# Performance work log

Hardware: AMD Instinct MI355X
Metric: run time of the kernel (lower is better)

## Reference

```python
import jax, jax.numpy as jnp
import numpy as np

B1, B2, CHUNK, HID, T = 64, 16, 128, 64, 131072
N_CHUNKS = 128


def setup_inputs() -> dict:
    key = jax.random.key(0)
    ks = jax.random.split(key, 12)
    # positive prices so log(p) is finite
    p = jax.random.uniform(ks[0], (T, 2), jnp.float32) * 2.0 + 0.5
    inds = jax.random.randint(ks[1], (B1,), 0, 100000, dtype=jnp.int32)
    open_slices = jax.random.randint(ks[2], (B1, B2, 1), 0, T, dtype=jnp.int32)
    ls_probs = jax.random.uniform(ks[3], (B1, B2, 1, 1), jnp.float32)
    open_probs = jax.random.uniform(ks[4], (B1, B2, 1, 1), jnp.float32)
    open_hx = jax.random.normal(ks[5], (B1, B2, 2, HID), jnp.float32) * 0.1
    s = 1.0 / np.sqrt(HID)
    # torch nn.LSTM params: gate order i,f,g,o
    W_ih = jax.random.uniform(ks[6], (4 * HID, 2), jnp.float32, -s, s)
    W_hh = jax.random.uniform(ks[7], (4 * HID, HID), jnp.float32, -s, s)
    b_ih = jax.random.uniform(ks[8], (4 * HID,), jnp.float32, -s, s)
    b_hh = jax.random.uniform(ks[9], (4 * HID,), jnp.float32, -s, s)
    W_out = jax.random.uniform(ks[10], (1, HID), jnp.float32, -s, s)
    b_out = jax.random.uniform(ks[11], (1,), jnp.float32, -s, s)
    return {"inds": inds, "p": p, "ls_probs": ls_probs, "open_probs": open_probs,
            "open_slices": open_slices, "open_hx": open_hx,
            "W_ih": W_ih, "W_hh": W_hh, "b_ih": b_ih, "b_hh": b_hh,
            "W_out": W_out, "b_out": b_out, "n_chunks": N_CHUNKS}


def reference(inds, p, ls_probs, open_probs, open_slices, open_hx,
              W_ih, W_hh, b_ih, b_hh, W_out, b_out, n_chunks):
    b1, b2 = open_hx.shape[:2]
    hid = open_hx.shape[-1]
    C = CHUNK
    h0 = open_hx[:, :, 0, :].reshape(b1 * b2, hid)
    c0 = open_hx[:, :, 1, :].reshape(b1 * b2, hid)
    open_logp = jnp.log(p[open_slices])  # (b1, b2, 1, 2)
    # sliding-window gather base: idx[i,j,t] = inds[i] + j + t (per-chunk offset added in scan)
    base = (inds[:, None, None]
            + jnp.arange(b2, dtype=inds.dtype)[None, :, None]
            + jnp.arange(C, dtype=inds.dtype)[None, None, :])  # (b1, b2, C)
    bias = b_ih + b_hh

    def lstm_chunk(x, h, c):  # x: (N, C, 2)
        xg = x @ W_ih.T + bias  # precompute input projection: (N, C, 4H)
        def step(carry, xg_t):
            h, c = carry
            g = xg_t + h @ W_hh.T
            i, f, gg, o = jnp.split(g, 4, axis=-1)
            c = jax.nn.sigmoid(f) * c + jax.nn.sigmoid(i) * jnp.tanh(gg)
            h = jax.nn.sigmoid(o) * jnp.tanh(c)
            return (h, c), h
        (h, c), hs = jax.lax.scan(step, (h, c), xg.swapaxes(0, 1))
        return hs.swapaxes(0, 1), h, c  # (N, C, H)

    def chunk_step(carry, offset):
        h, c, last_nd, loss = carry
        idx = base + offset * C                      # (b1, b2, C)
        p_chunk = p[idx]                             # (b1, b2, C, 2)
        x = p_chunk - p_chunk[:, :, :1, :]           # re-center on first step of chunk
        out, h, c = lstm_chunk(x.reshape(b1 * b2, C, 2), h, c)
        probs = jax.nn.sigmoid(out.reshape(b1, b2, C, hid) @ W_out.T + b_out)  # (b1,b2,C,1)
        not_done = last_nd * jnp.cumprod(1.0 - probs[:, :, :-1], axis=2)       # (b1,b2,C-1,1)
        probs = jnp.concatenate([probs[:, :, :1], probs[:, :, 1:] * not_done], axis=2)
        last_nd = not_done[:, :, -1:, :]
        logp = jnp.log(p_chunk)
        payoff = ls_probs * (logp - open_logp) + (1.0 - ls_probs) * (open_logp - logp)
        loss = loss + jnp.sum(open_probs * probs * payoff)
        return (h, c, last_nd, loss), None

    init = (h0, c0, jnp.ones((b1, b2, 1, 1), p.dtype), jnp.zeros((), p.dtype))
    (_, _, _, loss), _ = jax.lax.scan(chunk_step, init, jnp.arange(n_chunks))
    return loss
```

## Files before the change

### kernel.cpp

```cpp
#include <hip/hip_runtime.h>


#define CH  128
#define HID 64

typedef __fp16 half8 __attribute__((ext_vector_type(8)));
typedef float  f32x4 __attribute__((ext_vector_type(4)));
typedef int    int4v __attribute__((ext_vector_type(4)));

__device__ __forceinline__ float rlf(float v, int l) {
  return __builtin_bit_cast(float, __builtin_amdgcn_readlane(__builtin_bit_cast(int, v), l));
}
__device__ __forceinline__ int packh(float a, float b) {
  return __builtin_bit_cast(int, __builtin_amdgcn_cvt_pkrtz(a, b));
}
__device__ __forceinline__ float frcp(float x) { return __builtin_amdgcn_rcpf(x); }
__device__ __forceinline__ float sigm(float x) { return frcp(1.0f + __expf(-x)); }
__device__ __forceinline__ float tanh_(float x) {
  float e = __expf(2.0f * x);
  return 1.0f - 2.0f * frcp(e + 1.0f);
}
template <int CTRL, int RMASK>
__device__ __forceinline__ float dpp_add(float v) {
  int x = __builtin_amdgcn_update_dpp(0, __builtin_bit_cast(int, v), CTRL, RMASK, 0xF, true);
  return v + __builtin_bit_cast(float, x);
}
__device__ __forceinline__ float dpp_xor1(float v) {
  int x = __builtin_amdgcn_update_dpp(0, __builtin_bit_cast(int, v), 0xB1, 0xF, 0xF, true);
  return __builtin_bit_cast(float, x);
}
__device__ __forceinline__ float dpp_wave_sum(float v) {
  v = dpp_add<0x111, 0xF>(v);
  v = dpp_add<0x112, 0xF>(v);
  v = dpp_add<0x114, 0xF>(v);
  v = dpp_add<0x118, 0xF>(v);
  v = dpp_add<0x142, 0xA>(v);
  v = dpp_add<0x143, 0xC>(v);
  return v;
}

__global__ __attribute__((amdgpu_flat_work_group_size(128, 128), amdgpu_waves_per_eu(2, 2)))
void pc_lstm_kernel(const int* __restrict__ inds,
                    const float* __restrict__ p,
                    const float* __restrict__ ls_probs,
                    const float* __restrict__ open_probs,
                    const int* __restrict__ open_slices,
                    const float* __restrict__ open_hx,
                    const float* __restrict__ W_ih,
                    const float* __restrict__ W_hh,
                    const float* __restrict__ b_ih,
                    const float* __restrict__ b_hh,
                    const float* __restrict__ W_out,
                    const float* __restrict__ b_out,
                    const int* __restrict__ n_chunks_p,
                    float* __restrict__ out)
{
  __shared__ __fp16 ring[2][CH][HID];
  __shared__ int prod;
  __shared__ int cons;

  const int tid  = threadIdx.x;
  const int wv   = tid >> 6;
  const int lane = tid & 63;
  const int s    = blockIdx.x;
  const int n_chunks = n_chunks_p[0];
  const int tbase = inds[s >> 4] + (s & 15);
  const float2* p2 = (const float2*)p;

  if (tid == 0) { prod = 0; cons = 0; }
  __syncthreads();

  if (wv == 0) {
    const int kg = lane >> 4;
    const int cc = lane & 15;

    half8 Wb[32];
#pragma unroll
    for (int t = 0; t < 16; ++t) {
#pragma unroll
      for (int kc = 0; kc < 2; ++kc) {
        const float* wp = W_hh + (16 * t + cc) * HID + 32 * kc + 8 * kg;
        half8 w;
#pragma unroll
        for (int j = 0; j < 8; ++j) w[j] = (__fp16)wp[j];
        Wb[2 * t + kc] = w;
      }
    }

    float wxa[4], wxb[4], bb[4];
#pragma unroll
    for (int g = 0; g < 4; ++g) {
      const int r = g * HID + lane;
      wxa[g] = W_ih[2 * r];
      wxb[g] = W_ih[2 * r + 1];
      bb[g]  = b_ih[r] + b_hh[r];
    }
    float h = open_hx[(s * 2 + 0) * HID + lane];
    float c = open_hx[(s * 2 + 1) * HID + lane];

    int ia0[4], ia1[4];
#pragma unroll
    for (int w = 0; w < 4; ++w) {
      ia0[w] = 4 * (8 * kg + 2 * w);
      ia1[w] = 4 * (32 + 8 * kg + 2 * w);
    }

    const bool u1 = (lane & 16) != 0;
    const bool u2 = (lane & 32) != 0;
    const f32x4 zero4 = {0.f, 0.f, 0.f, 0.f};

    float2 curA = p2[tbase + lane];
    float2 curB = p2[tbase + HID + lane];
    float2 nxtA = curA, nxtB = curB;

    for (int off = 0; off < n_chunks; ++off) {
      if (off) { curA = nxtA; curB = nxtB; }
      const float px0 = rlf(curA.x, 0);
      const float px1 = rlf(curA.y, 0);
      float2 xA, xB;
      xA.x = curA.x - px0; xA.y = curA.y - px1;
      xB.x = curB.x - px0; xB.y = curB.y - px1;
      if (off + 1 < n_chunks) {
        const int nb = tbase + (off + 1) * CH;
        nxtA = p2[nb + lane];
        nxtB = p2[nb + HID + lane];
      }
      while (__hip_atomic_load(&cons, __ATOMIC_ACQUIRE, __HIP_MEMORY_SCOPE_WORKGROUP) + 2 <= off)
        __builtin_amdgcn_s_sleep(8);

      __fp16* slot = &ring[off & 1][0][0];
#pragma unroll
      for (int hf = 0; hf < 2; ++hf) {
        const float xcx = hf ? xB.x : xA.x;
        const float xcy = hf ? xB.y : xA.y;
#pragma unroll 1
        for (int tl = 0; tl < 64; ++tl) {
          const int hp = packh(h, dpp_xor1(h));
          int4v A0, A1;
#pragma unroll
          for (int w = 0; w < 4; ++w) {
            A0[w] = __builtin_amdgcn_ds_bpermute(ia0[w], hp);
            A1[w] = __builtin_amdgcn_ds_bpermute(ia1[w], hp);
          }
          const half8 a0 = __builtin_bit_cast(half8, A0);
          const half8 a1 = __builtin_bit_cast(half8, A1);

          const float x0 = rlf(xcx, tl);
          const float x1 = rlf(xcy, tl);

          float pa[4];
#pragma unroll
          for (int g = 0; g < 4; ++g) {
            f32x4 q0 = __builtin_amdgcn_mfma_f32_16x16x32_f16(a0, Wb[8 * g + 0], zero4, 0, 0, 0);
            q0       = __builtin_amdgcn_mfma_f32_16x16x32_f16(a1, Wb[8 * g + 1], q0,    0, 0, 0);
            f32x4 q1 = __builtin_amdgcn_mfma_f32_16x16x32_f16(a0, Wb[8 * g + 2], zero4, 0, 0, 0);
            q1       = __builtin_amdgcn_mfma_f32_16x16x32_f16(a1, Wb[8 * g + 3], q1,    0, 0, 0);
            f32x4 q2 = __builtin_amdgcn_mfma_f32_16x16x32_f16(a0, Wb[8 * g + 4], zero4, 0, 0, 0);
            q2       = __builtin_amdgcn_mfma_f32_16x16x32_f16(a1, Wb[8 * g + 5], q2,    0, 0, 0);
            f32x4 q3 = __builtin_amdgcn_mfma_f32_16x16x32_f16(a0, Wb[8 * g + 6], zero4, 0, 0, 0);
            q3       = __builtin_amdgcn_mfma_f32_16x16x32_f16(a1, Wb[8 * g + 7], q3,    0, 0, 0);
            const float s01 = u1 ? q1[0] : q0[0];
            const float s23 = u1 ? q3[0] : q2[0];
            const float dg  = u2 ? s23 : s01;
            pa[g] = fmaf(x0, wxa[g], fmaf(x1, wxb[g], dg + bb[g]));
          }

          const float ig = sigm(pa[0]);
          const float fg = sigm(pa[1]);
          const float gg = tanh_(pa[2]);
          const float og = sigm(pa[3]);
          c = fmaf(fg, c, ig * gg);
          h = og * tanh_(c);

          const int tt = hf * 64 + tl;
          slot[tt * HID + lane] = (__fp16)h;
        }
      }
      if (lane == 0)
        __hip_atomic_store(&prod, off + 1, __ATOMIC_RELEASE, __HIP_MEMORY_SCOPE_WORKGROUP);
    }
  } else {
    const float wo   = W_out[lane];
    const float bout = b_out[0];
    const int   os   = open_slices[s];
    const float OL   = __logf(p[2 * os]) + __logf(p[2 * os + 1]);
    const float coef = open_probs[s] * (2.0f * ls_probs[s] - 1.0f);

    float S = 1.0f, D = 1.0f, lsum = 0.0f, psum = 0.0f;

    for (int off = 0; off < n_chunks; ++off) {
      const int cb = tbase + off * CH;
      const float2 cA = p2[cb + lane];
      const float2 cB = p2[cb + HID + lane];
      const float LA = __logf(cA.x) + __logf(cA.y);
      const float LB = __logf(cB.x) + __logf(cB.y);

      while (__hip_atomic_load(&prod, __ATOMIC_ACQUIRE, __HIP_MEMORY_SCOPE_WORKGROUP) <= off)
        __builtin_amdgcn_s_sleep(32);

      const __fp16* slot = &ring[off & 1][0][0];
#pragma unroll 1
      for (int tt = 0; tt < CH; ++tt) {
        const float hv = (float)slot[tt * HID + lane];
        const float z  = rlf(dpp_wave_sum(hv * wo), 63);
        const float pr = sigm(z + bout);
        const float Lt = (tt < 64) ? rlf(LA, tt) : rlf(LB, tt - 64);
        const float pn = (tt == 0) ? pr : pr * D;
        lsum = fmaf(pn, Lt, lsum);
        psum += pn;
        if (tt == 0)           D = S * (1.0f - pr);
        else if (tt < CH - 1)  D *= (1.0f - pr);
        else                   S = D;
      }
      if (lane == 0)
        __hip_atomic_store(&cons, off + 1, __ATOMIC_RELEASE, __HIP_MEMORY_SCOPE_WORKGROUP);
    }
    if (lane == 0) atomicAdd(out, coef * (lsum - OL * psum));
  }
}

extern "C" void kernel_launch(void* const* d_in, const int* in_sizes, int n_in,
                              void* d_out, int out_size, void* d_ws, size_t ws_size,
                              hipStream_t stream) {
  (void)hipMemsetAsync(d_out, 0, sizeof(float), stream);

  pc_lstm_kernel<<<dim3(1024), dim3(128), 0, stream>>>(
      (const int*)d_in[0],
      (const float*)d_in[1],
      (const float*)d_in[2],
      (const float*)d_in[3],
      (const int*)d_in[4],
      (const float*)d_in[5],
      (const float*)d_in[6],
      (const float*)d_in[7],
      (const float*)d_in[8],
      (const float*)d_in[9],
      (const float*)d_in[10],
      (const float*)d_in[11],
      (const int*)d_in[12],
      (float*)d_out);
}
```

Measured before the change: 7.032 ms.

## Split LSTM gate matmuls across both waves with per-step LDS handshakes

The recurrent W_hh matmul is now divided between the two waves. Wave 0 computes the input and cell gates. Wave 1 computes the forget and output gates and also evaluates the output head one step behind. The gate values and h are exchanged every timestep through LDS, using tag-encoded 64-bit slots and a step counter with spin-waits. This replaces the old chunk-level producer/consumer ring. The aim is to halve the serial MFMA chain per timestep, at the cost of two cross-wave LDS round trips and busy-waiting on the critical path of every step.

```diff
diff --git a/kernel.cpp b/kernel.cpp
--- a/kernel.cpp
+++ b/kernel.cpp
@@ -7,6 +7,8 @@
 typedef __fp16 half8 __attribute__((ext_vector_type(8)));
 typedef float  f32x4 __attribute__((ext_vector_type(4)));
 typedef int    int4v __attribute__((ext_vector_type(4)));
+
+#define MFMA16(A, B, C) __builtin_amdgcn_mfma_f32_16x16x32_f16((A), (B), (C), 0, 0, 0)
 
 __device__ __forceinline__ float rlf(float v, int l) {
   return __builtin_bit_cast(float, __builtin_amdgcn_readlane(__builtin_bit_cast(int, v), l));
@@ -37,6 +39,10 @@
   v = dpp_add<0x142, 0xA>(v);
   v = dpp_add<0x143, 0xC>(v);
   return v;
+}
+__device__ __forceinline__ unsigned long long enc_tag(float v, int gs) {
+  const unsigned b = __builtin_bit_cast(unsigned, v);
+  return (unsigned long long)b | ((unsigned long long)(b ^ (unsigned)gs) << 32);
 }
 
 __global__ __attribute__((amdgpu_flat_work_group_size(128, 128), amdgpu_waves_per_eu(2, 2)))
@@ -55,46 +61,48 @@
                     const int* __restrict__ n_chunks_p,
                     float* __restrict__ out)
 {
-  __shared__ __fp16 ring[2][CH][HID];
-  __shared__ int prod;
-  __shared__ int cons;
+  __shared__ __fp16 hring[4][HID];
+  __shared__ unsigned long long commF[HID];
+  __shared__ unsigned long long commO[HID];
+  __shared__ int hflag;
 
   const int tid  = threadIdx.x;
   const int wv   = tid >> 6;
   const int lane = tid & 63;
   const int s    = blockIdx.x;
   const int n_chunks = n_chunks_p[0];
+  const int NSTEP = n_chunks * CH;
   const int tbase = inds[s >> 4] + (s & 15);
   const float2* p2 = (const float2*)p;
-
-  if (tid == 0) { prod = 0; cons = 0; }
+  const int kg = lane >> 4;
+  const int cc = lane & 15;
+  const bool u1 = (lane & 16) != 0;
+  const bool u2 = (lane & 32) != 0;
+  const f32x4 zero4 = {0.f, 0.f, 0.f, 0.f};
+
+  if (tid < HID) { commF[tid] = 0ull; commO[tid] = 0ull; }
+  if (tid == 0) hflag = -1;
   __syncthreads();
 
   if (wv == 0) {
-    const int kg = lane >> 4;
-    const int cc = lane & 15;
-
-    half8 Wb[32];
-#pragma unroll
-    for (int t = 0; t < 16; ++t) {
+    half8 Wb[16];
+#pragma unroll
+    for (int ti = 0; ti < 8; ++ti) {
+      const int t = (ti < 4) ? ti : ti + 4;
 #pragma unroll
       for (int kc = 0; kc < 2; ++kc) {
         const float* wp = W_hh + (16 * t + cc) * HID + 32 * kc + 8 * kg;
         half8 w;
 #pragma unroll
         for (int j = 0; j < 8; ++j) w[j] = (__fp16)wp[j];
-        Wb[2 * t + kc] = w;
-      }
-    }
-
-    float wxa[4], wxb[4], bb[4];
-#pragma unroll
-    for (int g = 0; g < 4; ++g) {
-      const int r = g * HID + lane;
-      wxa[g] = W_ih[2 * r];
-      wxb[g] = W_ih[2 * r + 1];
-      bb[g]  = b_ih[r] + b_hh[r];
-    }
+        Wb[2 * ti + kc] = w;
+      }
+    }
+    const float wxi0 = W_ih[2 * lane],                wxi1 = W_ih[2 * lane + 1];
+    const float bbi  = b_ih[lane] + b_hh[lane];
+    const float wxg0 = W_ih[2 * (2 * HID + lane)],    wxg1 = W_ih[2 * (2 * HID + lane) + 1];
+    const float bbg  = b_ih[2 * HID + lane] + b_hh[2 * HID + lane];
+
     float h = open_hx[(s * 2 + 0) * HID + lane];
     float c = open_hx[(s * 2 + 1) * HID + lane];
 
@@ -105,9 +113,10 @@
       ia1[w] = 4 * (32 + 8 * kg + 2 * w);
     }
 
-    const bool u1 = (lane & 16) != 0;
-    const bool u2 = (lane & 32) != 0;
-    const f32x4 zero4 = {0.f, 0.f, 0.f, 0.f};
+    int hp = packh(h, dpp_xor1(h));
+    ((unsigned short*)&hring[0][0])[lane] = (unsigned short)(hp & 0xffff);
+    asm volatile("" ::: "memory");
+    __hip_atomic_store(&hflag, 0, __ATOMIC_RELAXED, __HIP_MEMORY_SCOPE_WORKGROUP);
 
     float2 curA = p2[tbase + lane];
     float2 curB = p2[tbase + HID + lane];
@@ -125,61 +134,96 @@
         nxtA = p2[nb + lane];
         nxtB = p2[nb + HID + lane];
       }
-      while (__hip_atomic_load(&cons, __ATOMIC_ACQUIRE, __HIP_MEMORY_SCOPE_WORKGROUP) + 2 <= off)
-        __builtin_amdgcn_s_sleep(8);
-
-      __fp16* slot = &ring[off & 1][0][0];
 #pragma unroll
       for (int hf = 0; hf < 2; ++hf) {
         const float xcx = hf ? xB.x : xA.x;
         const float xcy = hf ? xB.y : xA.y;
 #pragma unroll 1
         for (int tl = 0; tl < 64; ++tl) {
-          const int hp = packh(h, dpp_xor1(h));
+          const int gs = off * CH + hf * 64 + tl + 1;
           int4v A0, A1;
 #pragma unroll
-          for (int w = 0; w < 4; ++w) {
-            A0[w] = __builtin_amdgcn_ds_bpermute(ia0[w], hp);
-            A1[w] = __builtin_amdgcn_ds_bpermute(ia1[w], hp);
-          }
+          for (int w = 0; w < 4; ++w) A0[w] = __builtin_amdgcn_ds_bpermute(ia0[w], hp);
+#pragma unroll
+          for (int w = 0; w < 4; ++w) A1[w] = __builtin_amdgcn_ds_bpermute(ia1[w], hp);
           const half8 a0 = __builtin_bit_cast(half8, A0);
           const half8 a1 = __builtin_bit_cast(half8, A1);
-
           const float x0 = rlf(xcx, tl);
           const float x1 = rlf(xcy, tl);
 
-          float pa[4];
-#pragma unroll
-          for (int g = 0; g < 4; ++g) {
-            f32x4 q0 = __builtin_amdgcn_mfma_f32_16x16x32_f16(a0, Wb[8 * g + 0], zero4, 0, 0, 0);
-            q0       = __builtin_amdgcn_mfma_f32_16x16x32_f16(a1, Wb[8 * g + 1], q0,    0, 0, 0);
-            f32x4 q1 = __builtin_amdgcn_mfma_f32_16x16x32_f16(a0, Wb[8 * g + 2], zero4, 0, 0, 0);
-            q1       = __builtin_amdgcn_mfma_f32_16x16x32_f16(a1, Wb[8 * g + 3], q1,    0, 0, 0);
-            f32x4 q2 = __builtin_amdgcn_mfma_f32_16x16x32_f16(a0, Wb[8 * g + 4], zero4, 0, 0, 0);
-            q2       = __builtin_amdgcn_mfma_f32_16x16x32_f16(a1, Wb[8 * g + 5], q2,    0, 0, 0);
-            f32x4 q3 = __builtin_amdgcn_mfma_f32_16x16x32_f16(a0, Wb[8 * g + 6], zero4, 0, 0, 0);
-            q3       = __builtin_amdgcn_mfma_f32_16x16x32_f16(a1, Wb[8 * g + 7], q3,    0, 0, 0);
-            const float s01 = u1 ? q1[0] : q0[0];
-            const float s23 = u1 ? q3[0] : q2[0];
-            const float dg  = u2 ? s23 : s01;
-            pa[g] = fmaf(x0, wxa[g], fmaf(x1, wxb[g], dg + bb[g]));
+          f32x4 q0 = MFMA16(a0, Wb[0],  zero4);
+          f32x4 q1 = MFMA16(a0, Wb[2],  zero4);
+          f32x4 q2 = MFMA16(a0, Wb[4],  zero4);
+          f32x4 q3 = MFMA16(a0, Wb[6],  zero4);
+          f32x4 s0 = MFMA16(a0, Wb[8],  zero4);
+          f32x4 s1 = MFMA16(a0, Wb[10], zero4);
+          f32x4 s2 = MFMA16(a0, Wb[12], zero4);
+          f32x4 s3 = MFMA16(a0, Wb[14], zero4);
+          q0 = MFMA16(a1, Wb[1],  q0);
+          q1 = MFMA16(a1, Wb[3],  q1);
+          q2 = MFMA16(a1, Wb[5],  q2);
+          q3 = MFMA16(a1, Wb[7],  q3);
+          s0 = MFMA16(a1, Wb[9],  s0);
+          s1 = MFMA16(a1, Wb[11], s1);
+          s2 = MFMA16(a1, Wb[13], s2);
+          s3 = MFMA16(a1, Wb[15], s3);
+
+          const float si01 = u1 ? q1[0] : q0[0];
+          const float si23 = u1 ? q3[0] : q2[0];
+          const float di   = u2 ? si23 : si01;
+          const float pai  = fmaf(x0, wxi0, fmaf(x1, wxi1, di + bbi));
+          const float ig   = sigm(pai);
+          const float sg01 = u1 ? s1[0] : s0[0];
+          const float sg23 = u1 ? s3[0] : s2[0];
+          const float dg   = u2 ? sg23 : sg01;
+          const float pag  = fmaf(x0, wxg0, fmaf(x1, wxg1, dg + bbg));
+          const float gg   = tanh_(pag);
+
+          float fg;
+          for (;;) {
+            const unsigned long long v =
+                __hip_atomic_load(&commF[lane], __ATOMIC_RELAXED, __HIP_MEMORY_SCOPE_WORKGROUP);
+            const unsigned lo = (unsigned)v, hi = (unsigned)(v >> 32);
+            if ((lo ^ hi) == (unsigned)gs) { fg = __builtin_bit_cast(float, lo); break; }
           }
-
-          const float ig = sigm(pa[0]);
-          const float fg = sigm(pa[1]);
-          const float gg = tanh_(pa[2]);
-          const float og = sigm(pa[3]);
           c = fmaf(fg, c, ig * gg);
-          h = og * tanh_(c);
-
-          const int tt = hf * 64 + tl;
-          slot[tt * HID + lane] = (__fp16)h;
+          const float tc = tanh_(c);
+
+          float og;
+          for (;;) {
+            const unsigned long long v =
+                __hip_atomic_load(&commO[lane], __ATOMIC_RELAXED, __HIP_MEMORY_SCOPE_WORKGROUP);
+            const unsigned lo = (unsigned)v, hi = (unsigned)(v >> 32);
+            if ((lo ^ hi) == (unsigned)gs) { og = __builtin_bit_cast(float, lo); break; }
+          }
+          h = og * tc;
+
+          hp = packh(h, dpp_xor1(h));
+          ((unsigned short*)&hring[gs & 3][0])[lane] = (unsigned short)(hp & 0xffff);
+          asm volatile("" ::: "memory");
+          __hip_atomic_store(&hflag, gs, __ATOMIC_RELAXED, __HIP_MEMORY_SCOPE_WORKGROUP);
         }
       }
-      if (lane == 0)
-        __hip_atomic_store(&prod, off + 1, __ATOMIC_RELEASE, __HIP_MEMORY_SCOPE_WORKGROUP);
     }
   } else {
+    half8 Wb[16];
+#pragma unroll
+    for (int ti = 0; ti < 8; ++ti) {
+      const int t = (ti < 4) ? (4 + ti) : (8 + ti);
+#pragma unroll
+      for (int kc = 0; kc < 2; ++kc) {
+        const float* wp = W_hh + (16 * t + cc) * HID + 32 * kc + 8 * kg;
+        half8 w;
+#pragma unroll
+        for (int j = 0; j < 8; ++j) w[j] = (__fp16)wp[j];
+        Wb[2 * ti + kc] = w;
+      }
+    }
+    const float wxf0 = W_ih[2 * (1 * HID + lane)], wxf1 = W_ih[2 * (1 * HID + lane) + 1];
+    const float bbf  = b_ih[1 * HID + lane] + b_hh[1 * HID + lane];
+    const float wxo0 = W_ih[2 * (3 * HID + lane)], wxo1 = W_ih[2 * (3 * HID + lane) + 1];
+    const float bbo  = b_ih[3 * HID + lane] + b_hh[3 * HID + lane];
+
     const float wo   = W_out[lane];
     const float bout = b_out[0];
     const int   os   = open_slices[s];
@@ -187,34 +231,100 @@
     const float coef = open_probs[s] * (2.0f * ls_probs[s] - 1.0f);
 
     float S = 1.0f, D = 1.0f, lsum = 0.0f, psum = 0.0f;
+    float LAc = 0.f, LBc = 0.f, LAp = 0.f, LBp = 0.f;
+
+    float2 curA = p2[tbase + lane];
+    float2 curB = p2[tbase + HID + lane];
+    float2 nxtA = curA, nxtB = curB;
 
     for (int off = 0; off < n_chunks; ++off) {
-      const int cb = tbase + off * CH;
-      const float2 cA = p2[cb + lane];
-      const float2 cB = p2[cb + HID + lane];
-      const float LA = __logf(cA.x) + __logf(cA.y);
-      const float LB = __logf(cB.x) + __logf(cB.y);
-
-      while (__hip_atomic_load(&prod, __ATOMIC_ACQUIRE, __HIP_MEMORY_SCOPE_WORKGROUP) <= off)
-        __builtin_amdgcn_s_sleep(32);
-
-      const __fp16* slot = &ring[off & 1][0][0];
+      if (off) { curA = nxtA; curB = nxtB; LAp = LAc; LBp = LBc; }
+      LAc = __logf(curA.x) + __logf(curA.y);
+      LBc = __logf(curB.x) + __logf(curB.y);
+      const float px0 = rlf(curA.x, 0);
+      const float px1 = rlf(curA.y, 0);
+      float2 xA, xB;
+      xA.x = curA.x - px0; xA.y = curA.y - px1;
+      xB.x = curB.x - px0; xB.y = curB.y - px1;
+      if (off + 1 < n_chunks) {
+        const int nb = tbase + (off + 1) * CH;
+        nxtA = p2[nb + lane];
+        nxtB = p2[nb + HID + lane];
+      }
+#pragma unroll
+      for (int hf = 0; hf < 2; ++hf) {
+        const float xcx = hf ? xB.x : xA.x;
+        const float xcy = hf ? xB.y : xA.y;
 #pragma unroll 1
-      for (int tt = 0; tt < CH; ++tt) {
-        const float hv = (float)slot[tt * HID + lane];
-        const float z  = rlf(dpp_wave_sum(hv * wo), 63);
-        const float pr = sigm(z + bout);
-        const float Lt = (tt < 64) ? rlf(LA, tt) : rlf(LB, tt - 64);
-        const float pn = (tt == 0) ? pr : pr * D;
-        lsum = fmaf(pn, Lt, lsum);
-        psum += pn;
-        if (tt == 0)           D = S * (1.0f - pr);
-        else if (tt < CH - 1)  D *= (1.0f - pr);
-        else                   S = D;
-      }
-      if (lane == 0)
-        __hip_atomic_store(&cons, off + 1, __ATOMIC_RELEASE, __HIP_MEMORY_SCOPE_WORKGROUP);
-    }
+        for (int tl = 0; tl < 64; ++tl) {
+          const int gs = off * CH + hf * 64 + tl + 1;
+          while (__hip_atomic_load(&hflag, __ATOMIC_RELAXED, __HIP_MEMORY_SCOPE_WORKGROUP) < gs - 1) {}
+          asm volatile("" ::: "memory");
+          const __fp16* prow = &hring[(gs - 1) & 3][0];
+          const half8 a0 = *(const half8*)((const char*)prow + 16 * kg);
+          const half8 a1 = *(const half8*)((const char*)prow + 64 + 16 * kg);
+          const float hv = (float)prow[lane];
+          const float x0 = rlf(xcx, tl);
+          const float x1 = rlf(xcy, tl);
+
+          f32x4 q0 = MFMA16(a0, Wb[0],  zero4);
+          f32x4 q1 = MFMA16(a0, Wb[2],  zero4);
+          f32x4 q2 = MFMA16(a0, Wb[4],  zero4);
+          f32x4 q3 = MFMA16(a0, Wb[6],  zero4);
+          q0 = MFMA16(a1, Wb[1],  q0);
+          q1 = MFMA16(a1, Wb[3],  q1);
+          q2 = MFMA16(a1, Wb[5],  q2);
+          q3 = MFMA16(a1, Wb[7],  q3);
+          f32x4 r0 = MFMA16(a0, Wb[8],  zero4);
+          f32x4 r1 = MFMA16(a0, Wb[10], zero4);
+          const float sf01 = u1 ? q1[0] : q0[0];
+          const float sf23 = u1 ? q3[0] : q2[0];
+          const float df   = u2 ? sf23 : sf01;
+          const float paf  = fmaf(x0, wxf0, fmaf(x1, wxf1, df + bbf));
+          const float fgv  = sigm(paf);
+          __hip_atomic_store(&commF[lane], enc_tag(fgv, gs),
+                             __ATOMIC_RELAXED, __HIP_MEMORY_SCOPE_WORKGROUP);
+          f32x4 r2 = MFMA16(a0, Wb[12], zero4);
+          f32x4 r3 = MFMA16(a0, Wb[14], zero4);
+          r0 = MFMA16(a1, Wb[9],  r0);
+          r1 = MFMA16(a1, Wb[11], r1);
+          r2 = MFMA16(a1, Wb[13], r2);
+          r3 = MFMA16(a1, Wb[15], r3);
+          const float so01 = u1 ? r1[0] : r0[0];
+          const float so23 = u1 ? r3[0] : r2[0];
+          const float dox  = u2 ? so23 : so01;
+          const float pao  = fmaf(x0, wxo0, fmaf(x1, wxo1, dox + bbo));
+          const float ogv  = sigm(pao);
+          __hip_atomic_store(&commO[lane], enc_tag(ogv, gs),
+                             __ATOMIC_RELAXED, __HIP_MEMORY_SCOPE_WORKGROUP);
+
+          if (gs >= 2) {
+            const int rp   = hf * 64 + tl - 1;
+            const float z  = rlf(dpp_wave_sum(hv * wo), 63);
+            const float pr = sigm(z + bout);
+            const int pos  = (rp < 0) ? (CH - 1) : rp;
+            const float LA_ = (rp < 0) ? LAp : LAc;
+            const float LB_ = (rp < 0) ? LBp : LBc;
+            const float Lt = (pos < 64) ? rlf(LA_, pos) : rlf(LB_, pos - 64);
+            const float pn = (pos == 0) ? pr : pr * D;
+            lsum = fmaf(pn, Lt, lsum);
+            psum += pn;
+            if (pos == 0)           D = S * (1.0f - pr);
+            else if (pos < CH - 1)  D *= (1.0f - pr);
+            else                    S = D;
+          }
+        }
+      }
+    }
+    while (__hip_atomic_load(&hflag, __ATOMIC_RELAXED, __HIP_MEMORY_SCOPE_WORKGROUP) < NSTEP) {}
+    asm volatile("" ::: "memory");
+    const float hvN = (float)hring[NSTEP & 3][lane];
+    const float zN  = rlf(dpp_wave_sum(hvN * wo), 63);
+    const float prN = sigm(zN + bout);
+    const float LtN = rlf(LBc, 63);
+    const float pnN = prN * D;
+    lsum = fmaf(pnN, LtN, lsum);
+    psum += pnN;
     if (lane == 0) atomicAdd(out, coef * (lsum - OL * psum));
   }
 }
```

New measurement: 8.978 ms. 27.7% more time.

## Split LSTM gates between MFMA and VALU FMAs with interleaved scheduling

Applied to the files above, without the earlier changes.

The recurrent step now computes only the i and f gate projections with MFMA. The g and o gates are computed in fp32 on the vector ALU, using readlane broadcasts of h and per-lane rows of W_hh held in registers. Sched barriers interleave the scalar FMAs between MFMA issues so both units work in parallel on the latency-bound serial recurrence. This halves the MFMA chain per timestep but adds 128 FMAs, 64 readlanes and a large register footprint, which risks spills or longer VALU latency.

```diff
diff --git a/kernel.cpp b/kernel.cpp
--- a/kernel.cpp
+++ b/kernel.cpp
@@ -7,6 +7,9 @@
 typedef __fp16 half8 __attribute__((ext_vector_type(8)));
 typedef float  f32x4 __attribute__((ext_vector_type(4)));
 typedef int    int4v __attribute__((ext_vector_type(4)));
+
+#define SB() __builtin_amdgcn_sched_barrier(0)
+#define MFMA16(A, B, C) __builtin_amdgcn_mfma_f32_16x16x32_f16((A), (B), (C), 0, 0, 0)
 
 __device__ __forceinline__ float rlf(float v, int l) {
   return __builtin_bit_cast(float, __builtin_amdgcn_readlane(__builtin_bit_cast(int, v), l));
@@ -74,9 +77,9 @@
     const int kg = lane >> 4;
     const int cc = lane & 15;
 
-    half8 Wb[32];
-#pragma unroll
-    for (int t = 0; t < 16; ++t) {
+    half8 Wb[16];
+#pragma unroll
+    for (int t = 0; t < 8; ++t) {
 #pragma unroll
       for (int kc = 0; kc < 2; ++kc) {
         const float* wp = W_hh + (16 * t + cc) * HID + 32 * kc + 8 * kg;
@@ -84,6 +87,18 @@
 #pragma unroll
         for (int j = 0; j < 8; ++j) w[j] = (__fp16)wp[j];
         Wb[2 * t + kc] = w;
+      }
+    }
+
+    float Wg[64], Wo[64];
+    {
+      const float4* rg = (const float4*)(W_hh + (2 * HID + lane) * HID);
+      const float4* ro = (const float4*)(W_hh + (3 * HID + lane) * HID);
+#pragma unroll
+      for (int j = 0; j < 16; ++j) {
+        const float4 vg = rg[j], vo = ro[j];
+        Wg[4 * j] = vg.x; Wg[4 * j + 1] = vg.y; Wg[4 * j + 2] = vg.z; Wg[4 * j + 3] = vg.w;
+        Wo[4 * j] = vo.x; Wo[4 * j + 1] = vo.y; Wo[4 * j + 2] = vo.z; Wo[4 * j + 3] = vo.w;
       }
     }
 
@@ -112,6 +127,14 @@
     float2 curA = p2[tbase + lane];
     float2 curB = p2[tbase + HID + lane];
     float2 nxtA = curA, nxtB = curB;
+
+#define GO4(R) { \
+    const float s0_ = rlf(h, 4 * (R) + 0), s1_ = rlf(h, 4 * (R) + 1); \
+    const float s2_ = rlf(h, 4 * (R) + 2), s3_ = rlf(h, 4 * (R) + 3); \
+    ga = fmaf(s0_, Wg[4 * (R) + 0], ga);  oa = fmaf(s0_, Wo[4 * (R) + 0], oa); \
+    gb = fmaf(s1_, Wg[4 * (R) + 1], gb);  ob = fmaf(s1_, Wo[4 * (R) + 1], ob); \
+    ga = fmaf(s2_, Wg[4 * (R) + 2], ga);  oa = fmaf(s2_, Wo[4 * (R) + 2], oa); \
+    gb = fmaf(s3_, Wg[4 * (R) + 3], gb);  ob = fmaf(s3_, Wo[4 * (R) + 3], ob); } SB()
 
     for (int off = 0; off < n_chunks; ++off) {
       if (off) { curA = nxtA; curB = nxtB; }
@@ -138,37 +161,75 @@
           const int hp = packh(h, dpp_xor1(h));
           int4v A0, A1;
 #pragma unroll
-          for (int w = 0; w < 4; ++w) {
-            A0[w] = __builtin_amdgcn_ds_bpermute(ia0[w], hp);
-            A1[w] = __builtin_amdgcn_ds_bpermute(ia1[w], hp);
-          }
+          for (int w = 0; w < 4; ++w) A0[w] = __builtin_amdgcn_ds_bpermute(ia0[w], hp);
+#pragma unroll
+          for (int w = 0; w < 4; ++w) A1[w] = __builtin_amdgcn_ds_bpermute(ia1[w], hp);
           const half8 a0 = __builtin_bit_cast(half8, A0);
           const half8 a1 = __builtin_bit_cast(half8, A1);
-
           const float x0 = rlf(xcx, tl);
           const float x1 = rlf(xcy, tl);
 
-          float pa[4];
-#pragma unroll
-          for (int g = 0; g < 4; ++g) {
-            f32x4 q0 = __builtin_amdgcn_mfma_f32_16x16x32_f16(a0, Wb[8 * g + 0], zero4, 0, 0, 0);
-            q0       = __builtin_amdgcn_mfma_f32_16x16x32_f16(a1, Wb[8 * g + 1], q0,    0, 0, 0);
-            f32x4 q1 = __builtin_amdgcn_mfma_f32_16x16x32_f16(a0, Wb[8 * g + 2], zero4, 0, 0, 0);
-            q1       = __builtin_amdgcn_mfma_f32_16x16x32_f16(a1, Wb[8 * g + 3], q1,    0, 0, 0);
-            f32x4 q2 = __builtin_amdgcn_mfma_f32_16x16x32_f16(a0, Wb[8 * g + 4], zero4, 0, 0, 0);
-            q2       = __builtin_amdgcn_mfma_f32_16x16x32_f16(a1, Wb[8 * g + 5], q2,    0, 0, 0);
-            f32x4 q3 = __builtin_amdgcn_mfma_f32_16x16x32_f16(a0, Wb[8 * g + 6], zero4, 0, 0, 0);
-            q3       = __builtin_amdgcn_mfma_f32_16x16x32_f16(a1, Wb[8 * g + 7], q3,    0, 0, 0);
-            const float s01 = u1 ? q1[0] : q0[0];
-            const float s23 = u1 ? q3[0] : q2[0];
-            const float dg  = u2 ? s23 : s01;
-            pa[g] = fmaf(x0, wxa[g], fmaf(x1, wxb[g], dg + bb[g]));
+          float ga = fmaf(x0, wxa[2], bb[2]);
+          float gb = x1 * wxb[2];
+          float oa = fmaf(x0, wxa[3], bb[3]);
+          float ob = x1 * wxb[3];
+          float ei = 0.0f;
+          SB();
+
+          f32x4 t0 = MFMA16(a0, Wb[0],  zero4); GO4(0);
+          t0       = MFMA16(a1, Wb[1],  t0);    GO4(1);
+          f32x4 t1 = MFMA16(a0, Wb[2],  zero4); GO4(2);
+          t1       = MFMA16(a1, Wb[3],  t1);    GO4(3);
+          f32x4 t2 = MFMA16(a0, Wb[4],  zero4); GO4(4);
+          t2       = MFMA16(a1, Wb[5],  t2);    GO4(5);
+          f32x4 t3 = MFMA16(a0, Wb[6],  zero4); GO4(6);
+          t3       = MFMA16(a1, Wb[7],  t3);    GO4(7);
+
+          f32x4 t4 = MFMA16(a0, Wb[8],  zero4);
+          {
+            const float si01 = u1 ? t1[0] : t0[0];
+            const float si23 = u1 ? t3[0] : t2[0];
+            const float di   = u2 ? si23 : si01;
+            const float pai  = fmaf(x0, wxa[0], fmaf(x1, wxb[0], di + bb[0]));
+            ei = __expf(-pai);
+            const float s0_ = rlf(h, 32), s1_ = rlf(h, 33);
+            ga = fmaf(s0_, Wg[32], ga);  oa = fmaf(s0_, Wo[32], oa);
+            gb = fmaf(s1_, Wg[33], gb);  ob = fmaf(s1_, Wo[33], ob);
           }
-
-          const float ig = sigm(pa[0]);
-          const float fg = sigm(pa[1]);
-          const float gg = tanh_(pa[2]);
-          const float og = sigm(pa[3]);
+          SB();
+          t4 = MFMA16(a1, Wb[9], t4);
+          {
+            const float s0_ = rlf(h, 34), s1_ = rlf(h, 35);
+            const float s2_ = rlf(h, 36), s3_ = rlf(h, 37);
+            ga = fmaf(s0_, Wg[34], ga);  oa = fmaf(s0_, Wo[34], oa);
+            gb = fmaf(s1_, Wg[35], gb);  ob = fmaf(s1_, Wo[35], ob);
+            ga = fmaf(s2_, Wg[36], ga);  oa = fmaf(s2_, Wo[36], oa);
+            gb = fmaf(s3_, Wg[37], gb);  ob = fmaf(s3_, Wo[37], ob);
+          }
+          SB();
+          f32x4 t5 = MFMA16(a0, Wb[10], zero4);
+          {
+            const float s0_ = rlf(h, 38), s1_ = rlf(h, 39);
+            ga = fmaf(s0_, Wg[38], ga);  oa = fmaf(s0_, Wo[38], oa);
+            gb = fmaf(s1_, Wg[39], gb);  ob = fmaf(s1_, Wo[39], ob);
+          }
+          SB();
+          t5 = MFMA16(a1, Wb[11], t5);    GO4(10);
+          f32x4 t6 = MFMA16(a0, Wb[12], zero4); GO4(11);
+          t6 = MFMA16(a1, Wb[13], t6);    GO4(12);
+          f32x4 t7 = MFMA16(a0, Wb[14], zero4); GO4(13);
+          t7 = MFMA16(a1, Wb[15], t7);    GO4(14);
+          GO4(15);
+
+          const float eg   = __expf(2.0f * (ga + gb));
+          const float og   = sigm(oa + ob);
+          const float sf01 = u1 ? t5[0] : t4[0];
+          const float sf23 = u1 ? t7[0] : t6[0];
+          const float df   = u2 ? sf23 : sf01;
+          const float paf  = fmaf(x0, wxa[1], fmaf(x1, wxb[1], df + bb[1]));
+          const float fg   = sigm(paf);
+          const float ig   = frcp(1.0f + ei);
+          const float gg   = 1.0f - 2.0f * frcp(eg + 1.0f);
           c = fmaf(fg, c, ig * gg);
           h = og * tanh_(c);
 
@@ -179,6 +240,7 @@
       if (lane == 0)
         __hip_atomic_store(&prod, off + 1, __ATOMIC_RELEASE, __HIP_MEMORY_SCOPE_WORKGROUP);
     }
+#undef GO4
   } else {
     const float wo   = W_out[lane];
     const float bout = b_out[0];
```

Measured after the change: 9.159 ms. 30.2% more time.
